# Kernel optimization log

Measured on AMD Instinct MI355X. Metric: run time of the kernel, lower is better.

The kernel has to match this reference:

```python
import jax, jax.numpy as jnp
import numpy as np

N = 8   # num_channels
K = 4   # number of mixture components
B = 2097152  # voxels (128^3 volume)
LOG_2PI = float(np.log(2.0 * np.pi))


def _diag_tril_indices(n):
    # position of diagonal elements within the row-major lower-tri flattening
    # matches diag_elem(): 0, 2, 5, 9, ...
    return np.cumsum(np.arange(n) + 1) - 1


def setup_inputs() -> dict:
    key = jax.random.key(0)
    k1, k2, k3, k4 = jax.random.split(key, 4)
    tri = N * (N + 1) // 2
    x = jax.random.normal(k1, (B, N), dtype=jnp.float32)
    weights = jax.random.normal(k2, (K,), dtype=jnp.float32)
    loc = jax.random.normal(k3, (N, K), dtype=jnp.float32)
    sp = jax.random.normal(k4, (tri, K), dtype=jnp.float32) * 0.1
    d = _diag_tril_indices(N)
    sp = sp.at[d].set(jnp.abs(sp[d]) + 0.5)  # valid lower-Cholesky: positive diag
    return {"x": x, "weights": weights, "loc": loc, "scale_params": sp}


def reference(x, weights, loc, scale_params):
    # Scatter packed tril params into K lower-triangular scale matrices [K, N, N]
    rows, cols = np.tril_indices(N)
    L = jnp.zeros((K, N, N), dtype=x.dtype).at[:, rows, cols].set(scale_params.T)

    # Centered data per cluster: [K, N, B]
    diff = jnp.swapaxes(x[None, :, :] - loc.T[:, None, :], 1, 2)
    # Whiten: z = L^{-1} (x - mu), batched over K -> [K, N, B]
    z = jax.lax.linalg.triangular_solve(L, diff, left_side=True, lower=True)
    maha = jnp.sum(z * z, axis=1)  # [K, B]

    log_det = jnp.sum(jnp.log(jnp.diagonal(L, axis1=1, axis2=2)), axis=1)  # [K]
    log_p = -0.5 * (maha + N * LOG_2PI) - log_det[:, None]  # [K, B]

    log_w = jax.nn.log_softmax(weights)  # [K]
    # stable weighted mixture logsumexp over clusters -> [B]
    return jax.scipy.special.logsumexp(log_p + log_w[:, None], axis=0)
```

## Files before the change

kernel.cpp:

```cpp
#include <hip/hip_runtime.h>
#include <math.h>

#define NCH 8
#define KMIX 4
#define TRI 36
#define CSTRIDE 48
#define LOG_2PI 1.8378770664093453f

__global__ void gmm_setup(const float* __restrict__ weights,
                          const float* __restrict__ loc,
                          const float* __restrict__ sp,
                          float* __restrict__ ws) {
    int k = threadIdx.x;
    if (k >= KMIX) return;

    float wmax = weights[0];
    for (int i = 1; i < KMIX; ++i) wmax = fmaxf(wmax, weights[i]);
    float se = 0.f;
    for (int i = 0; i < KMIX; ++i) se += expf(weights[i] - wmax);
    float logw = weights[k] - (wmax + logf(se));

    float L[NCH][NCH];
    int t = 0;
    for (int i = 0; i < NCH; ++i)
        for (int j = 0; j <= i; ++j)
            L[i][j] = sp[t++ * KMIX + k];

    float logdet = 0.f;
    for (int i = 0; i < NCH; ++i) logdet += logf(L[i][i]);

    float Li[NCH][NCH];
    for (int j = 0; j < NCH; ++j) {
        for (int i = j; i < NCH; ++i) {
            float s = (i == j) ? 1.f : 0.f;
            for (int m = j; m < i; ++m) s -= L[i][m] * Li[m][j];
            Li[i][j] = s / L[i][i];
        }
    }

    float mu[NCH];
    for (int j = 0; j < NCH; ++j) mu[j] = loc[j * KMIX + k];

    float* o = ws + k * CSTRIDE;
    t = 0;
    for (int i = 0; i < NCH; ++i)
        for (int j = 0; j <= i; ++j)
            o[t++] = Li[i][j];
    for (int i = 0; i < NCH; ++i) {
        float b = 0.f;
        for (int j = 0; j <= i; ++j) b += Li[i][j] * mu[j];
        o[TRI + i] = b;
    }
    o[44] = logw - logdet - 0.5f * NCH * LOG_2PI;
}

__global__ __launch_bounds__(256) void gmm_main(const float* __restrict__ x,
                                                const float* __restrict__ cst,
                                                float* __restrict__ out,
                                                int B) {
    int v = blockIdx.x * blockDim.x + threadIdx.x;
    if (v >= B) return;

    const float4* xp = reinterpret_cast<const float4*>(x + (size_t)v * NCH);
    float4 a0 = xp[0];
    float4 a1 = xp[1];
    float xv[NCH] = {a0.x, a0.y, a0.z, a0.w, a1.x, a1.y, a1.z, a1.w};

    float lp[KMIX];
#pragma unroll
    for (int k = 0; k < KMIX; ++k) {
        const float* c = cst + k * CSTRIDE;
        float maha = 0.f;
        int t = 0;
#pragma unroll
        for (int i = 0; i < NCH; ++i) {
            float z = -c[TRI + i];
#pragma unroll
            for (int j = 0; j <= i; ++j) {
                z = fmaf(c[t], xv[j], z);
                ++t;
            }
            maha = fmaf(z, z, maha);
        }
        lp[k] = fmaf(-0.5f, maha, c[44]);
    }

    float mx = fmaxf(fmaxf(lp[0], lp[1]), fmaxf(lp[2], lp[3]));
    float s = __expf(lp[0] - mx) + __expf(lp[1] - mx) +
              __expf(lp[2] - mx) + __expf(lp[3] - mx);
    out[v] = mx + __logf(s);
}

extern "C" void kernel_launch(void* const* d_in, const int* in_sizes, int n_in,
                              void* d_out, int out_size, void* d_ws, size_t ws_size,
                              hipStream_t stream) {
    const float* x       = (const float*)d_in[0];
    const float* weights = (const float*)d_in[1];
    const float* loc     = (const float*)d_in[2];
    const float* sp      = (const float*)d_in[3];
    float* out = (float*)d_out;
    float* ws  = (float*)d_ws;

    int B = in_sizes[0] / NCH;

    gmm_setup<<<1, 64, 0, stream>>>(weights, loc, sp, ws);

    int threads = 256;
    int blocks = (B + threads - 1) / threads;
    gmm_main<<<blocks, threads, 0, stream>>>(x, ws, out, B);
}
```

Baseline: 26.70 us.

## Fuse setup into main kernel with per-wave mixture component and LDS reduction

Removes the separate setup launch: each block recomputes the Cholesky inverse and constants itself, one wavefront per mixture component, and holds them in scalar registers via readfirstlane. Each wave evaluates its component for 256 voxels, then the per-component log-probs are exchanged through LDS for the logsumexp. A fixed grid of 2048 blocks loops over voxels. This cuts one launch and the global constant loads, but each voxel's x is now read by all four waves and every iteration adds barriers.

```diff
diff --git a/kernel.cpp b/kernel.cpp
--- a/kernel.cpp
+++ b/kernel.cpp
@@ -4,91 +4,128 @@
 #define NCH 8
 #define KMIX 4
 #define TRI 36
-#define CSTRIDE 48
 #define LOG_2PI 1.8378770664093453f
 
-__global__ void gmm_setup(const float* __restrict__ weights,
-                          const float* __restrict__ loc,
-                          const float* __restrict__ sp,
-                          float* __restrict__ ws) {
-    int k = threadIdx.x;
-    if (k >= KMIX) return;
+__device__ __forceinline__ float sgpr_f(float v) {
+    return __uint_as_float(__builtin_amdgcn_readfirstlane(__float_as_uint(v)));
+}
 
-    float wmax = weights[0];
-    for (int i = 1; i < KMIX; ++i) wmax = fmaxf(wmax, weights[i]);
-    float se = 0.f;
-    for (int i = 0; i < KMIX; ++i) se += expf(weights[i] - wmax);
-    float logw = weights[k] - (wmax + logf(se));
+__global__ __launch_bounds__(256) void gmm_fused(const float* __restrict__ x,
+                                                 const float* __restrict__ weights,
+                                                 const float* __restrict__ loc,
+                                                 const float* __restrict__ sp,
+                                                 float* __restrict__ out,
+                                                 int B, int nIter) {
+    __shared__ float lp_lds[KMIX][256];
+
+    const int tid  = threadIdx.x;
+    const int wid  = tid >> 6;
+    const int lane = tid & 63;
+    const int k    = wid;
+
+    float w0 = weights[0], w1 = weights[1], w2 = weights[2], w3 = weights[3];
+    float wk = (k == 0) ? w0 : (k == 1) ? w1 : (k == 2) ? w2 : w3;
+    float wmax = fmaxf(fmaxf(w0, w1), fmaxf(w2, w3));
+    float se = expf(w0 - wmax) + expf(w1 - wmax) + expf(w2 - wmax) + expf(w3 - wmax);
+    float logw = wk - (wmax + logf(se));
 
     float L[NCH][NCH];
-    int t = 0;
-    for (int i = 0; i < NCH; ++i)
-        for (int j = 0; j <= i; ++j)
-            L[i][j] = sp[t++ * KMIX + k];
-
+    {
+        int t = 0;
+#pragma unroll
+        for (int i = 0; i < NCH; ++i)
+#pragma unroll
+            for (int j = 0; j <= i; ++j)
+                L[i][j] = sp[t++ * KMIX + k];
+    }
     float logdet = 0.f;
+#pragma unroll
     for (int i = 0; i < NCH; ++i) logdet += logf(L[i][i]);
 
     float Li[NCH][NCH];
-    for (int j = 0; j < NCH; ++j) {
+#pragma unroll
+    for (int j = 0; j < NCH; ++j)
+#pragma unroll
         for (int i = j; i < NCH; ++i) {
             float s = (i == j) ? 1.f : 0.f;
-            for (int m = j; m < i; ++m) s -= L[i][m] * Li[m][j];
+#pragma unroll
+            for (int m = 0; m < NCH; ++m)
+                if (m >= j && m < i) s -= L[i][m] * Li[m][j];
             Li[i][j] = s / L[i][i];
         }
-    }
 
     float mu[NCH];
+#pragma unroll
     for (int j = 0; j < NCH; ++j) mu[j] = loc[j * KMIX + k];
 
-    float* o = ws + k * CSTRIDE;
-    t = 0;
-    for (int i = 0; i < NCH; ++i)
-        for (int j = 0; j <= i; ++j)
-            o[t++] = Li[i][j];
-    for (int i = 0; i < NCH; ++i) {
-        float b = 0.f;
-        for (int j = 0; j <= i; ++j) b += Li[i][j] * mu[j];
-        o[TRI + i] = b;
-    }
-    o[44] = logw - logdet - 0.5f * NCH * LOG_2PI;
-}
-
-__global__ __launch_bounds__(256) void gmm_main(const float* __restrict__ x,
-                                                const float* __restrict__ cst,
-                                                float* __restrict__ out,
-                                                int B) {
-    int v = blockIdx.x * blockDim.x + threadIdx.x;
-    if (v >= B) return;
-
-    const float4* xp = reinterpret_cast<const float4*>(x + (size_t)v * NCH);
-    float4 a0 = xp[0];
-    float4 a1 = xp[1];
-    float xv[NCH] = {a0.x, a0.y, a0.z, a0.w, a1.x, a1.y, a1.z, a1.w};
-
-    float lp[KMIX];
-#pragma unroll
-    for (int k = 0; k < KMIX; ++k) {
-        const float* c = cst + k * CSTRIDE;
-        float maha = 0.f;
+    float sLi[TRI], sNb[NCH];
+    {
         int t = 0;
 #pragma unroll
         for (int i = 0; i < NCH; ++i) {
-            float z = -c[TRI + i];
+            float b = 0.f;
 #pragma unroll
             for (int j = 0; j <= i; ++j) {
-                z = fmaf(c[t], xv[j], z);
+                sLi[t] = sgpr_f(Li[i][j]);
+                b += Li[i][j] * mu[j];
                 ++t;
             }
-            maha = fmaf(z, z, maha);
+            sNb[i] = sgpr_f(-b);
         }
-        lp[k] = fmaf(-0.5f, maha, c[44]);
     }
+    const float sC = sgpr_f(logw - logdet - 0.5f * NCH * LOG_2PI);
 
-    float mx = fmaxf(fmaxf(lp[0], lp[1]), fmaxf(lp[2], lp[3]));
-    float s = __expf(lp[0] - mx) + __expf(lp[1] - mx) +
-              __expf(lp[2] - mx) + __expf(lp[3] - mx);
-    out[v] = mx + __logf(s);
+    const int base0 = blockIdx.x * (256 * nIter);
+    for (int it = 0; it < nIter; ++it) {
+        const int vbase = base0 + it * 256;
+
+        float lpv[4];
+#pragma unroll
+        for (int s = 0; s < 4; ++s) {
+            const int v = vbase + s * 64 + lane;
+            float xv[NCH];
+            if (v < B) {
+                const float4* xp = reinterpret_cast<const float4*>(x + (size_t)v * NCH);
+                float4 a0 = xp[0], a1 = xp[1];
+                xv[0] = a0.x; xv[1] = a0.y; xv[2] = a0.z; xv[3] = a0.w;
+                xv[4] = a1.x; xv[5] = a1.y; xv[6] = a1.z; xv[7] = a1.w;
+            } else {
+#pragma unroll
+                for (int i = 0; i < NCH; ++i) xv[i] = 0.f;
+            }
+            float maha = 0.f;
+            int t = 0;
+#pragma unroll
+            for (int i = 0; i < NCH; ++i) {
+                float z = sNb[i];
+#pragma unroll
+                for (int j = 0; j <= i; ++j) {
+                    z = fmaf(sLi[t], xv[j], z);
+                    ++t;
+                }
+                maha = fmaf(z, z, maha);
+            }
+            lpv[s] = fmaf(-0.5f, maha, sC);
+        }
+
+        __syncthreads();
+#pragma unroll
+        for (int s = 0; s < 4; ++s) lp_lds[k][s * 64 + lane] = lpv[s];
+        __syncthreads();
+
+        {
+            const int vo = wid * 64 + lane;
+            const int v  = vbase + vo;
+            float l0 = lp_lds[0][vo], l1 = lp_lds[1][vo];
+            float l2 = lp_lds[2][vo], l3 = lp_lds[3][vo];
+            if (v < B) {
+                float mx = fmaxf(fmaxf(l0, l1), fmaxf(l2, l3));
+                float s2 = __expf(l0 - mx) + __expf(l1 - mx) +
+                           __expf(l2 - mx) + __expf(l3 - mx);
+                out[v] = mx + __logf(s2);
+            }
+        }
+    }
 }
 
 extern "C" void kernel_launch(void* const* d_in, const int* in_sizes, int n_in,
@@ -99,13 +136,11 @@
     const float* loc     = (const float*)d_in[2];
     const float* sp      = (const float*)d_in[3];
     float* out = (float*)d_out;
-    float* ws  = (float*)d_ws;
 
-    int B = in_sizes[0] / NCH;
+    const int B = in_sizes[0] / NCH;
 
-    gmm_setup<<<1, 64, 0, stream>>>(weights, loc, sp, ws);
+    const int blocks = 2048;
+    const int nIter  = (B + 256 * blocks - 1) / (256 * blocks);
 
-    int threads = 256;
-    int blocks = (B + threads - 1) / threads;
-    gmm_main<<<blocks, threads, 0, stream>>>(x, ws, out, B);
+    gmm_fused<<<blocks, 256, 0, stream>>>(x, weights, loc, sp, out, B, nIter);
 }
```

After: 32.63 us. 1.22x slower.
